# Optimization experiments

Hardware: AMD Instinct MI355X
Metric: run time of the kernel (lower is better)

Reference implementation:

```python
import math
import jax, jax.numpy as jnp
import numpy as np

SEGMENT_LENGTHS = [1024, 2048, 4096]
DILATION_RATES = [1, 2, 4]


def _head_groups(num_heads, num_segments):
    base = num_heads // num_segments
    extra = num_heads % num_segments
    groups = [base] * num_segments
    for i in range(extra):
        groups[-(i + 1)] += 1
    return groups


def _dilated_indices(n, segment_len, dilation_rate, offset):
    # Mirrors RingDilatedAttentionV3._apply_dilated_pattern (static shapes -> numpy)
    if dilation_rate == 1:
        return np.arange(n, dtype=np.int32)
    out = []
    for start in range(0, n, segment_len):
        seg = np.arange(start, min(start + segment_len, n), dtype=np.int32)
        if len(seg) >= dilation_rate:
            dil = seg[offset::dilation_rate]
            while len(dil) < len(seg):
                dil = np.concatenate([dil, seg[: len(seg) - len(dil)]])
            out.append(dil[: len(seg)])
        else:
            out.append(seg)
    return np.concatenate(out)


def _build_head_indices(n, h):
    # [h, n] gather indices along the sequence dim, one row per head
    groups = _head_groups(h, len(SEGMENT_LENGTHS))
    rows = []
    for i, (s, r, g) in enumerate(zip(SEGMENT_LENGTHS, DILATION_RATES, groups)):
        idx = _dilated_indices(n, s, r, offset=i)
        rows.extend([idx] * g)
    return np.stack(rows)


def setup_inputs() -> dict:
    key = jax.random.key(0)
    kq, kk, kv = jax.random.split(key, 3)
    b, n, h, d = 1, 4096, 12, 64
    q = jax.random.normal(kq, (b, n, h, d), dtype=jnp.float32)
    k = jax.random.normal(kk, (b, n, h, d), dtype=jnp.float32)
    v = jax.random.normal(kv, (b, n, h, d), dtype=jnp.float32)
    return {"q": q, "k": k, "v": v}


def reference(q, k, v):
    b, n, h, d = q.shape
    idx = jnp.asarray(_build_head_indices(n, h))  # [h, n], static

    # (b, n, h, d) -> (b, h, n, d)
    qt = jnp.transpose(q, (0, 2, 1, 3))
    kt = jnp.transpose(k, (0, 2, 1, 3))
    vt = jnp.transpose(v, (0, 2, 1, 3))

    # Dilated gather along sequence, per head
    gather_idx = idx[None, :, :, None]  # [1, h, n, 1]
    kt = jnp.take_along_axis(kt, gather_idx, axis=2)
    vt = jnp.take_along_axis(vt, gather_idx, axis=2)

    scale = 1.0 / math.sqrt(d)
    scores = jnp.einsum("bhqd,bhkd->bhqk", qt, kt) * scale  # [b, h, n, n]
    attn = jax.nn.softmax(scores, axis=-1)
    out = jnp.einsum("bhqk,bhkd->bhqd", attn, vt)
    return jnp.transpose(out, (0, 2, 1, 3))  # (b, n, h, d)
```

## Files before the change

kernel.cpp:

```cpp
#include <hip/hip_runtime.h>
#include <hip/hip_bf16.h>
#include <math.h>


#define NQ 4096
#define NH 12
#define DD 64
#define KV 64
#define NT (NQ / KV)
#define PSTR 36
#define TILE_USHORT (KV * DD)
#define TILE_BYTES  (KV * DD * 2)
#define EXP2 __builtin_amdgcn_exp2f

typedef __attribute__((ext_vector_type(8))) short bf16x8;
typedef __attribute__((ext_vector_type(4))) float f32x4;
typedef __attribute__((ext_vector_type(4))) unsigned int u32x4;

__device__ __forceinline__ int map_src(int h, int j) {
    if (h < 4) {
        return j;
    } else if (h < 8) {
        int p = j & 2047;
        int base = j & ~2047;
        return base + (p < 1024 ? 1 + 2 * p : p - 1024);
    } else {
        return (j < 1024) ? (2 + 4 * j) : (j - 1024);
    }
}

__device__ __forceinline__ unsigned pk2(float lo, float hi) {
    __hip_bfloat162 t = __float22bfloat162_rn(float2{lo, hi});
    union { __hip_bfloat162 h; unsigned u; } c;
    c.h = t;
    return c.u;
}

__device__ __forceinline__ int swz(int row, int p) {
    return row * PSTR + (p ^ (((row >> 2) & 7) << 2));
}

__device__ __forceinline__ void gload16(const void* g, void* l) {
    __builtin_amdgcn_global_load_lds(
        (const __attribute__((address_space(1))) unsigned int*)g,
        (__attribute__((address_space(3))) unsigned int*)l, 16, 0, 0);
}

__global__ __launch_bounds__(256) void prepack(
    const float* __restrict__ k, const float* __restrict__ v,
    unsigned short* __restrict__ kp, unsigned short* __restrict__ vp)
{
    __shared__ float vt[KV][DD + 1];
    const int t = blockIdx.x, h = blockIdx.y, tid = threadIdx.x;
    const int row = tid >> 2, q4 = tid & 3;
    const int src = map_src(h, t * KV + row);

    {
        const float* kr = k + ((size_t)src * NH + h) * DD + 16 * q4;
        float4 a = *(const float4*)(kr + 0);
        float4 b = *(const float4*)(kr + 4);
        float4 c = *(const float4*)(kr + 8);
        float4 d = *(const float4*)(kr + 12);
        unsigned* kb = (unsigned*)(kp + (size_t)(h * NT + t) * TILE_USHORT);
        const int x = (row & 7) << 2;
        u32x4 w0, w1;
        w0.x = pk2(a.x, a.y); w0.y = pk2(a.z, a.w);
        w0.z = pk2(b.x, b.y); w0.w = pk2(b.z, b.w);
        w1.x = pk2(c.x, c.y); w1.y = pk2(c.z, c.w);
        w1.z = pk2(d.x, d.y); w1.w = pk2(d.z, d.w);
        *(u32x4*)(kb + (row << 5) + ((8 * q4) ^ x))     = w0;
        *(u32x4*)(kb + (row << 5) + ((8 * q4 + 4) ^ x)) = w1;
    }
    {
        const float* vr = v + ((size_t)src * NH + h) * DD + 16 * q4;
        #pragma unroll
        for (int i = 0; i < 16; ++i) vt[row][16 * q4 + i] = vr[i];
    }
    __syncthreads();
    {
        const int d = row, u = q4;
        unsigned* vb = (unsigned*)(vp + (size_t)(h * NT + t) * TILE_USHORT);
        const int x = (d & 7) << 2;
        u32x4 w0, w1;
        w0.x = pk2(vt[16*u +  0][d], vt[16*u +  1][d]);
        w0.y = pk2(vt[16*u +  2][d], vt[16*u +  3][d]);
        w0.z = pk2(vt[16*u +  4][d], vt[16*u +  5][d]);
        w0.w = pk2(vt[16*u +  6][d], vt[16*u +  7][d]);
        w1.x = pk2(vt[16*u +  8][d], vt[16*u +  9][d]);
        w1.y = pk2(vt[16*u + 10][d], vt[16*u + 11][d]);
        w1.z = pk2(vt[16*u + 12][d], vt[16*u + 13][d]);
        w1.w = pk2(vt[16*u + 14][d], vt[16*u + 15][d]);
        *(u32x4*)(vb + (d << 5) + ((8 * u) ^ x))     = w0;
        *(u32x4*)(vb + (d << 5) + ((8 * u + 4) ^ x)) = w1;
    }
}

__global__ __launch_bounds__(256, 2) void attn_mfma(
    const float* __restrict__ q,
    const unsigned short* __restrict__ kp,
    const unsigned short* __restrict__ vp,
    float* __restrict__ out)
{
    __shared__ __align__(16) unsigned short KsB[2][TILE_USHORT];
    __shared__ __align__(16) unsigned short VtB[2][TILE_USHORT];
    __shared__ __align__(16) unsigned short Ps[4 * 16 * PSTR * 2];

    const int h    = blockIdx.y;
    const int qblk = blockIdx.x;
    const int tid  = threadIdx.x;
    const int wave = tid >> 6;
    const int lane = tid & 63;
    const int lq   = lane & 15;
    const int g    = lane >> 4;
    const int xk   = (lq & 7) << 2;

    const int qi = qblk * 64 + wave * 16 + lq;

    const char* ksrc = (const char*)(kp + (size_t)h * NT * TILE_USHORT);
    const char* vsrc = (const char*)(vp + (size_t)h * NT * TILE_USHORT);
    const int lbase = wave * 2048;
    const int csrc  = lbase + lane * 16;

    const float qscale = 0.125f * 1.4426950408889634f;
    union { bf16x8 v8; unsigned u[4]; } qf[2];
    {
        const float* qp = q + ((size_t)qi * NH + h) * DD;
        #pragma unroll
        for (int ks = 0; ks < 2; ++ks) {
            float4 a = *(const float4*)(qp + 32 * ks + 8 * g);
            float4 b = *(const float4*)(qp + 32 * ks + 8 * g + 4);
            qf[ks].u[0] = pk2(a.x * qscale, a.y * qscale);
            qf[ks].u[1] = pk2(a.z * qscale, a.w * qscale);
            qf[ks].u[2] = pk2(b.x * qscale, b.y * qscale);
            qf[ks].u[3] = pk2(b.z * qscale, b.w * qscale);
        }
    }

    f32x4 o[4];
    #pragma unroll
    for (int mf = 0; mf < 4; ++mf) o[mf] = f32x4{0.f, 0.f, 0.f, 0.f};
    float m = -INFINITY, l = 0.f;

    unsigned* Pw = (unsigned*)Ps + wave * 16 * PSTR;

    gload16(ksrc + csrc,        (char*)KsB[0] + lbase);
    gload16(ksrc + csrc + 1024, (char*)KsB[0] + lbase + 1024);
    gload16(vsrc + csrc,        (char*)VtB[0] + lbase);
    gload16(vsrc + csrc + 1024, (char*)VtB[0] + lbase + 1024);

    for (int tile = 0; tile < NT; ++tile) {
        const int cur = tile & 1;
        __syncthreads();

        if (tile + 1 < NT) {
            const size_t nb = (size_t)(tile + 1) * TILE_BYTES;
            gload16(ksrc + nb + csrc,        (char*)KsB[cur ^ 1] + lbase);
            gload16(ksrc + nb + csrc + 1024, (char*)KsB[cur ^ 1] + lbase + 1024);
            gload16(vsrc + nb + csrc,        (char*)VtB[cur ^ 1] + lbase);
            gload16(vsrc + nb + csrc + 1024, (char*)VtB[cur ^ 1] + lbase + 1024);
        }

        const unsigned short* Ksc = KsB[cur];
        const unsigned short* Vtc = VtB[cur];

        f32x4 s[4];
        #pragma unroll
        for (int mf = 0; mf < 4; ++mf) {
            s[mf] = f32x4{0.f, 0.f, 0.f, 0.f};
            #pragma unroll
            for (int ks = 0; ks < 2; ++ks) {
                bf16x8 kf = *(const bf16x8*)(Ksc + 2 * (((16 * mf + lq) << 5) + ((4 * g + 16 * ks) ^ xk)));
                s[mf] = __builtin_amdgcn_mfma_f32_16x16x32_bf16(kf, qf[ks].v8, s[mf], 0, 0, 0);
            }
        }

        float u0 = fmaxf(fmaxf(s[0].x, s[0].y), s[0].z);
        float u1 = fmaxf(fmaxf(s[0].w, s[1].x), s[1].y);
        float u2 = fmaxf(fmaxf(s[1].z, s[1].w), s[2].x);
        float u3 = fmaxf(fmaxf(s[2].y, s[2].z), s[2].w);
        float u4 = fmaxf(fmaxf(s[3].x, s[3].y), s[3].z);
        float tm = fmaxf(fmaxf(fmaxf(u0, u1), u2),
                         fmaxf(fmaxf(u3, u4), s[3].w));
        tm = fmaxf(tm, __shfl_xor(tm, 16));
        tm = fmaxf(tm, __shfl_xor(tm, 32));
        if (__any(tm > m)) {
            float mn = fmaxf(m, tm);
            float sc = EXP2(m - mn);
            m = mn;
            l *= sc;
            #pragma unroll
            for (int mf = 0; mf < 4; ++mf) o[mf] *= sc;
        }
        #pragma unroll
        for (int mf = 0; mf < 4; ++mf) {
            f32x4 p;
            p.x = EXP2(s[mf].x - m);
            p.y = EXP2(s[mf].y - m);
            p.z = EXP2(s[mf].z - m);
            p.w = EXP2(s[mf].w - m);
            l += (p.x + p.y) + (p.z + p.w);
            Pw[swz(lq, 8 * mf + 2 * g + 0)] = pk2(p.x, p.y);
            Pw[swz(lq, 8 * mf + 2 * g + 1)] = pk2(p.z, p.w);
        }

        bf16x8 pf0 = *(const bf16x8*)((const unsigned short*)(Pw + swz(lq, 4 * g)));
        bf16x8 pf1 = *(const bf16x8*)((const unsigned short*)(Pw + swz(lq, 4 * g + 16)));
        #pragma unroll
        for (int mf = 0; mf < 4; ++mf) {
            const int vr = 16 * mf + lq;
            bf16x8 vf0 = *(const bf16x8*)(Vtc + 2 * ((vr << 5) + ((4 * g) ^ xk)));
            o[mf] = __builtin_amdgcn_mfma_f32_16x16x32_bf16(vf0, pf0, o[mf], 0, 0, 0);
            bf16x8 vf1 = *(const bf16x8*)(Vtc + 2 * ((vr << 5) + ((4 * g + 16) ^ xk)));
            o[mf] = __builtin_amdgcn_mfma_f32_16x16x32_bf16(vf1, pf1, o[mf], 0, 0, 0);
        }
    }

    l += __shfl_xor(l, 16);
    l += __shfl_xor(l, 32);
    float inv = 1.f / l;
    float* op = out + ((size_t)qi * NH + h) * DD;
    #pragma unroll
    for (int mf = 0; mf < 4; ++mf) {
        f32x4 r = o[mf] * inv;
        *(f32x4*)(op + 16 * mf + 4 * g) = r;
    }
}

extern "C" void kernel_launch(void* const* d_in, const int* in_sizes, int n_in,
                              void* d_out, int out_size, void* d_ws, size_t ws_size,
                              hipStream_t stream) {
    const float* q = (const float*)d_in[0];
    const float* k = (const float*)d_in[1];
    const float* v = (const float*)d_in[2];
    float* out     = (float*)d_out;

    unsigned short* kp = (unsigned short*)d_ws;
    unsigned short* vp = kp + (size_t)NH * NT * TILE_USHORT;

    prepack<<<dim3(NT, NH), 256, 0, stream>>>(k, v, kp, vp);
    attn_mfma<<<dim3(NQ / 64, NH), 256, 0, stream>>>(q, kp, vp, out);
}
```

Baseline: 178.7 us.

## Keep P in registers for PV via 16x16x16 MFMA, remap blocks across XCDs

The softmax probabilities are packed straight into registers and fed to 16x16x16 bf16 MFMAs, so the LDS round trip through the P scratch buffer and its extra reads go away. The grid is flattened and block IDs are remapped so that neighbouring blocks of one head land on the same XCD, which should improve L2 reuse of that head's K/V tiles. Launch bounds ask for 3 blocks per CU. The trade-off is twice as many MFMA instructions at half depth, plus more register pressure under the tighter occupancy target.

```diff
diff --git a/kernel.cpp b/kernel.cpp
--- a/kernel.cpp
+++ b/kernel.cpp
@@ -8,12 +8,12 @@
 #define DD 64
 #define KV 64
 #define NT (NQ / KV)
-#define PSTR 36
 #define TILE_USHORT (KV * DD)
 #define TILE_BYTES  (KV * DD * 2)
 #define EXP2 __builtin_amdgcn_exp2f
 
 typedef __attribute__((ext_vector_type(8))) short bf16x8;
+typedef __attribute__((ext_vector_type(4))) short bf16x4;
 typedef __attribute__((ext_vector_type(4))) float f32x4;
 typedef __attribute__((ext_vector_type(4))) unsigned int u32x4;
 
@@ -36,8 +36,17 @@
     return c.u;
 }
 
-__device__ __forceinline__ int swz(int row, int p) {
-    return row * PSTR + (p ^ (((row >> 2) & 7) << 2));
+__device__ __forceinline__ f32x4 mfma16(bf16x4 a, bf16x4 b, f32x4 c) {
+#if __has_builtin(__builtin_amdgcn_mfma_f32_16x16x16_bf16)
+    return __builtin_amdgcn_mfma_f32_16x16x16_bf16(a, b, c, 0, 0, 0);
+#elif __has_builtin(__builtin_amdgcn_mfma_f32_16x16x16bf16_1k)
+    return __builtin_amdgcn_mfma_f32_16x16x16bf16_1k(a, b, c, 0, 0, 0);
+#else
+    f32x4 d;
+    asm volatile("v_mfma_f32_16x16x16_bf16 %0, %1, %2, %3"
+                 : "=v"(d) : "v"(a), "v"(b), "v"(c));
+    return d;
+#endif
 }
 
 __device__ __forceinline__ void gload16(const void* g, void* l) {
@@ -95,7 +104,7 @@
     }
 }
 
-__global__ __launch_bounds__(256, 2) void attn_mfma(
+__global__ __launch_bounds__(256, 3) void attn_mfma(
     const float* __restrict__ q,
     const unsigned short* __restrict__ kp,
     const unsigned short* __restrict__ vp,
@@ -103,10 +112,12 @@
 {
     __shared__ __align__(16) unsigned short KsB[2][TILE_USHORT];
     __shared__ __align__(16) unsigned short VtB[2][TILE_USHORT];
-    __shared__ __align__(16) unsigned short Ps[4 * 16 * PSTR * 2];
-
-    const int h    = blockIdx.y;
-    const int qblk = blockIdx.x;
+
+    const int bid  = blockIdx.x;
+    const int virt = (bid & 7) * 96 + (bid >> 3);
+    const int h    = virt >> 6;
+    const int qblk = virt & 63;
+
     const int tid  = threadIdx.x;
     const int wave = tid >> 6;
     const int lane = tid & 63;
@@ -138,10 +149,8 @@
 
     f32x4 o[4];
     #pragma unroll
-    for (int mf = 0; mf < 4; ++mf) o[mf] = f32x4{0.f, 0.f, 0.f, 0.f};
+    for (int mo = 0; mo < 4; ++mo) o[mo] = f32x4{0.f, 0.f, 0.f, 0.f};
     float m = -INFINITY, l = 0.f;
-
-    unsigned* Pw = (unsigned*)Ps + wave * 16 * PSTR;
 
     gload16(ksrc + csrc,        (char*)KsB[0] + lbase);
     gload16(ksrc + csrc + 1024, (char*)KsB[0] + lbase + 1024);
@@ -161,7 +170,7 @@
         }
 
         const unsigned short* Ksc = KsB[cur];
-        const unsigned short* Vtc = VtB[cur];
+        const unsigned* Vtd = (const unsigned*)VtB[cur];
 
         f32x4 s[4];
         #pragma unroll
@@ -189,8 +198,9 @@
             m = mn;
             l *= sc;
             #pragma unroll
-            for (int mf = 0; mf < 4; ++mf) o[mf] *= sc;
-        }
+            for (int mo = 0; mo < 4; ++mo) o[mo] *= sc;
+        }
+        union { unsigned u[2]; bf16x4 h; } pf[4];
         #pragma unroll
         for (int mf = 0; mf < 4; ++mf) {
             f32x4 p;
@@ -199,19 +209,18 @@
             p.z = EXP2(s[mf].z - m);
             p.w = EXP2(s[mf].w - m);
             l += (p.x + p.y) + (p.z + p.w);
-            Pw[swz(lq, 8 * mf + 2 * g + 0)] = pk2(p.x, p.y);
-            Pw[swz(lq, 8 * mf + 2 * g + 1)] = pk2(p.z, p.w);
-        }
-
-        bf16x8 pf0 = *(const bf16x8*)((const unsigned short*)(Pw + swz(lq, 4 * g)));
-        bf16x8 pf1 = *(const bf16x8*)((const unsigned short*)(Pw + swz(lq, 4 * g + 16)));
+            pf[mf].u[0] = pk2(p.x, p.y);
+            pf[mf].u[1] = pk2(p.z, p.w);
+        }
+
         #pragma unroll
         for (int mf = 0; mf < 4; ++mf) {
-            const int vr = 16 * mf + lq;
-            bf16x8 vf0 = *(const bf16x8*)(Vtc + 2 * ((vr << 5) + ((4 * g) ^ xk)));
-            o[mf] = __builtin_amdgcn_mfma_f32_16x16x32_bf16(vf0, pf0, o[mf], 0, 0, 0);
-            bf16x8 vf1 = *(const bf16x8*)(Vtc + 2 * ((vr << 5) + ((4 * g + 16) ^ xk)));
-            o[mf] = __builtin_amdgcn_mfma_f32_16x16x32_bf16(vf1, pf1, o[mf], 0, 0, 0);
+            #pragma unroll
+            for (int mo = 0; mo < 4; ++mo) {
+                const int vr = 16 * mo + lq;
+                bf16x4 vf = *(const bf16x4*)(Vtd + ((vr << 5) + ((8 * mf + 2 * g) ^ xk)));
+                o[mo] = mfma16(vf, pf[mf].h, o[mo]);
+            }
         }
     }
 
@@ -220,9 +229,9 @@
     float inv = 1.f / l;
     float* op = out + ((size_t)qi * NH + h) * DD;
     #pragma unroll
-    for (int mf = 0; mf < 4; ++mf) {
-        f32x4 r = o[mf] * inv;
-        *(f32x4*)(op + 16 * mf + 4 * g) = r;
+    for (int mo = 0; mo < 4; ++mo) {
+        f32x4 r = o[mo] * inv;
+        *(f32x4*)(op + 16 * mo + 4 * g) = r;
     }
 }
 
@@ -238,5 +247,5 @@
     unsigned short* vp = kp + (size_t)NH * NT * TILE_USHORT;
 
     prepack<<<dim3(NT, NH), 256, 0, stream>>>(k, v, kp, vp);
-    attn_mfma<<<dim3(NQ / 64, NH), 256, 0, stream>>>(q, kp, vp, out);
-}
+    attn_mfma<<<dim3(NT * NH), 256, 0, stream>>>(q, kp, vp, out);
+}
```

Result: no change. 176.8 us (-1.1%).
